# Kernel tuning notes

Hardware: AMD Instinct MI355X
Metric: run time of the kernel (lower is better)

The kernel has to match this reference:

```python
import jax, jax.numpy as jnp
import numpy as np

B, S, W, SYM, HID, ENT, ROLE, VOCAB, MAXSEQ = 256, 30, 10, 128, 512, 64, 32, 64, 16
LAYERS = 3
EPS = 1e-6


def setup_inputs() -> dict:
    key = jax.random.key(0)
    ks = jax.random.split(key, 16)
    rn = lambda i, shape, s: jax.random.normal(ks[i], shape, dtype=jnp.float32) * s
    inp = {
        'story': jax.random.randint(ks[0], (B, S, W), 0, VOCAB),
        'query': jax.random.randint(ks[1], (B, W), 0, VOCAB),
        'word_embed': rn(2, (VOCAB, SYM), 0.1),
        'pos_embed': jnp.ones((MAXSEQ, SYM), jnp.float32) / MAXSEQ,
        'ue_W1': rn(3, (2, SYM, HID), 0.05), 'ue_b1': jnp.zeros((2, HID), jnp.float32),
        'ue_W2': rn(4, (2, HID, ENT), 0.05), 'ue_b2': jnp.zeros((2, ENT), jnp.float32),
        'ur_W1': rn(5, (3, SYM, HID), 0.05), 'ur_b1': jnp.zeros((3, HID), jnp.float32),
        'ur_W2': rn(6, (3, HID, ROLE), 0.05), 'ur_b2': jnp.zeros((3, ROLE), jnp.float32),
        'fwm': rn(7, (ENT, ROLE, ENT), 0.08),
        'ie_W1': rn(8, (2, SYM, HID), 0.05), 'ie_b1': jnp.zeros((2, HID), jnp.float32),
        'ie_W2': rn(9, (2, HID, ENT), 0.05), 'ie_b2': jnp.zeros((2, ENT), jnp.float32),
        'ir_W1': rn(10, (3, SYM, HID), 0.05), 'ir_b1': jnp.zeros((3, HID), jnp.float32),
        'ir_W2': rn(11, (3, HID, ROLE), 0.05), 'ir_b2': jnp.zeros((3, ROLE), jnp.float32),
        'ln_gain': jnp.ones((3, ENT), jnp.float32),
        'ln_bias': jnp.zeros((3, ENT), jnp.float32),
        'Z': rn(12, (ENT, 9), 0.1),
    }
    return inp


def reference(story, query, word_embed, pos_embed,
              ue_W1, ue_b1, ue_W2, ue_b2, ur_W1, ur_b1, ur_W2, ur_b2, fwm,
              ie_W1, ie_b1, ie_W2, ie_b2, ir_W1, ir_b1, ir_W2, ir_b2,
              ln_gain, ln_bias, Z):
    # ---- InputModule: embed + position-weighted word sum ----
    sent = jnp.einsum('bswe,we->bse', word_embed[story], pos_embed[:story.shape[2]])  # [B,S,SYM]
    q = jnp.einsum('bwe,we->be', word_embed[query], pos_embed[:query.shape[1]])       # [B,SYM]

    # ---- UpdateModule: 2-layer tanh MLPs (stacked over head index n) ----
    h = jnp.tanh(jnp.einsum('bse,neh->nbsh', sent, ue_W1) + ue_b1[:, None, None, :])
    eo = jnp.tanh(jnp.einsum('nbsh,nho->nbso', h, ue_W2) + ue_b2[:, None, None, :])
    e1, e2 = eo[0], eo[1]                                                             # [B,S,ENT]
    h = jnp.tanh(jnp.einsum('bse,neh->nbsh', sent, ur_W1) + ur_b1[:, None, None, :])
    ro = jnp.tanh(jnp.einsum('nbsh,nho->nbso', h, ur_W2) + ur_b2[:, None, None, :])
    r1, r2, r3 = ro[0], ro[1], ro[2]                                                  # [B,S,ROLE]

    paw = jnp.einsum('bsr,bsf->bsrf', r1, e2)  # partial_add_w
    pab = jnp.einsum('bsr,bsf->bsrf', r3, e1)  # partial_add_b
    tpr = jnp.broadcast_to(fwm, (story.shape[0],) + fwm.shape)  # [B,ENT,ROLE,ENT]

    def step(tpr, _):
        w_hat = jnp.einsum('bse,bsr,berf->bsf', e1, r1, tpr)
        tpr = tpr + jnp.einsum('bse,bsrf->berf', e1, paw - jnp.einsum('bsr,bsf->bsrf', r1, w_hat))
        m_hat = jnp.einsum('bse,bsr,berf->bsf', e1, r2, tpr)
        move_op = jnp.einsum('bsr,bsf->bsrf', r2, w_hat) - jnp.einsum('bsr,bsf->bsrf', r2, m_hat)
        tpr = tpr + jnp.einsum('bse,bsrf->berf', e1, move_op)
        b_hat = jnp.einsum('bse,bsr,berf->bsf', e2, r3, tpr)
        tpr = tpr + jnp.einsum('bse,bsrf->berf', e2, pab - jnp.einsum('bsr,bsf->bsrf', r3, b_hat))
        fn = jnp.sqrt(jnp.sum(tpr * tpr, axis=(1, 2, 3)))
        fn = jax.nn.relu(fn - 1.0) + 1.0
        return tpr / fn[:, None, None, None], None

    tpr, _ = jax.lax.scan(step, tpr, None, length=LAYERS)

    # ---- InferenceModule ----
    h = jnp.tanh(jnp.einsum('be,neh->nbh', q, ie_W1) + ie_b1[:, None, :])
    qeo = jnp.tanh(jnp.einsum('nbh,nho->nbo', h, ie_W2) + ie_b2[:, None, :])
    qe1 = qeo[0]
    h = jnp.tanh(jnp.einsum('be,neh->nbh', q, ir_W1) + ir_b1[:, None, :])
    qro = jnp.tanh(jnp.einsum('nbh,nho->nbo', h, ir_W2) + ir_b2[:, None, :])
    qr1, qr2, qr3 = qro[0], qro[1], qro[2]

    def ln(x, i):
        m = jnp.mean(x, -1, keepdims=True)
        s = jnp.std(x, -1, keepdims=True, ddof=1)
        return ln_gain[i] * (x - m) / (s + EPS) + ln_bias[i]

    i1 = ln(jnp.einsum('be,br,berf->bf', qe1, qr1, tpr), 0)
    i2 = ln(jnp.einsum('be,br,berf->bf', i1, qr2, tpr), 1)
    i3 = ln(jnp.einsum('be,br,berf->bf', i2, qr3, tpr), 2)
    return jnp.einsum('bf,fl->bl', i1 + i2 + i3, Z)  # [B,9]
```

## Files before the change

### kernel.cpp

```cpp
#include <hip/hip_runtime.h>
#include <hip/hip_bf16.h>

#define NB 256
#define NS 30
#define NW 10
#define SYM 128
#define HID 512
#define ENT 64
#define ROLE 32

typedef unsigned short ushortT;
typedef __attribute__((ext_vector_type(8))) short short8v;
typedef __attribute__((ext_vector_type(4))) float f32x4;

static const size_t OF_SENTB = 0;
static const size_t OF_QEMBB = 491520;
static const size_t OF_W1A   = 507904;
static const size_t OF_W2TE  = 802816;
static const size_t OF_W2TR  = 851968;
static const size_t OF_FWMB  = 901120;
static const size_t OF_E1    = 966656;
static const size_t OF_R1    = 1949696;
static const size_t OF_QE1   = 2686976;
static const size_t OF_QR1   = 2703360;
static const size_t OF_PP    = 2727936;
static const size_t OF_FN2   = 4202496;
static const size_t OF_G     = 4202624;

__device__ __forceinline__ ushortT f2bf(float x) {
  unsigned u = __float_as_uint(x);
  unsigned r = (u + 0x7fffu + ((u >> 16) & 1u)) >> 16;
  return (ushortT)r;
}
__device__ __forceinline__ float ftanh(float x) {
  float t = __expf(2.f * x);
  return 1.f - 2.f * __builtin_amdgcn_rcpf(t + 1.f);
}
__device__ __forceinline__ float dot4(const float4& a, const float4& b) {
  return a.x * b.x + a.y * b.y + a.z * b.z + a.w * b.w;
}
__device__ __forceinline__ float wreduce64(float v) {
  #pragma unroll
  for (int o = 32; o > 0; o >>= 1) v += __shfl_xor(v, o);
  return v;
}

__global__ __launch_bounds__(256) void prep_k(
    const int* __restrict__ story, const int* __restrict__ query,
    const float* __restrict__ WE, const float* __restrict__ PE,
    const float* __restrict__ ueW1, const float* __restrict__ urW1,
    const float* __restrict__ ieW1, const float* __restrict__ irW1,
    const float* __restrict__ ueW2, const float* __restrict__ urW2,
    const float* __restrict__ ieW2, const float* __restrict__ irW2,
    const float* __restrict__ fwm,
    ushortT* __restrict__ sentb, ushortT* __restrict__ qembb,
    ushortT* __restrict__ W1A, ushortT* __restrict__ W2TE,
    ushortT* __restrict__ W2TR, ushortT* __restrict__ fwmBT,
    float* __restrict__ fn2) {
  __shared__ float tl[64 * 65];
  __shared__ float red[4];
  int bx = blockIdx.x, tid = threadIdx.x;
  if (bx < 3968) {
    int row = bx * 2 + (tid >> 7);
    int e = tid & 127;
    const int* idx; ushortT* dst;
    if (row < 7680) { idx = story + (size_t)row * NW; dst = sentb + (size_t)row * SYM; }
    else            { idx = query + (size_t)(row - 7680) * NW; dst = qembb + (size_t)(row - 7680) * SYM; }
    float acc = 0.f;
    #pragma unroll
    for (int w = 0; w < NW; ++w) acc += WE[idx[w] * SYM + e] * PE[w * SYM + e];
    dst[e] = f2bf(acc);
    return;
  }
  bx -= 3968;
  const float* src; ushortT* dst; int R, C, tr0, tc0;
  if (bx < 144) {
    int h = bx >> 4, t = bx & 15;
    src = (h < 2) ? ueW1 + (size_t)h * 65536 : (h < 5) ? urW1 + (size_t)(h - 2) * 65536
        : (h == 5) ? ieW1 : irW1 + (size_t)(h - 6) * 65536;
    dst = W1A + (size_t)h * 65536;
    R = 128; C = 512; tr0 = (t >> 3) * 64; tc0 = (t & 7) * 64;
  } else if (bx < 168) {
    int h = (bx - 144) >> 3, t = (bx - 144) & 7;
    src = (h < 2) ? ueW2 + (size_t)h * 32768 : ieW2;
    dst = W2TE + (size_t)h * 32768;
    R = 512; C = 64; tr0 = t * 64; tc0 = 0;
  } else if (bx < 216) {
    int h = (bx - 168) >> 3, t = (bx - 168) & 7;
    src = (h < 3) ? urW2 + (size_t)h * 16384 : irW2 + (size_t)(h - 3) * 16384;
    dst = W2TR + (size_t)h * 16384;
    R = 512; C = 32; tr0 = t * 64; tc0 = 0;
  } else if (bx < 248) {
    int t = bx - 216;
    src = fwm; dst = fwmBT; R = 2048; C = 64; tr0 = t * 64; tc0 = 0;
  } else {
    int blk = bx - 248;
    const float4* f4 = reinterpret_cast<const float4*>(fwm) + blk * 4096;
    float a = 0.f;
    for (int i = tid; i < 4096; i += 256) {
      float4 v = f4[i];
      a += v.x*v.x + v.y*v.y + v.z*v.z + v.w*v.w;
    }
    a = wreduce64(a);
    if ((tid & 63) == 0) red[tid >> 6] = a;
    __syncthreads();
    if (tid == 0) fn2[blk] = red[0] + red[1] + red[2] + red[3];
    return;
  }
  int TC = (C < 64) ? C : 64;
  int n = 64 * TC;
  for (int i = tid; i < n; i += 256) {
    int r = i / TC, c = i % TC;
    tl[r * 65 + c] = src[(size_t)(tr0 + r) * C + tc0 + c];
  }
  __syncthreads();
  for (int i = tid; i < n; i += 256) {
    int c = i >> 6, r = i & 63;
    dst[(size_t)(tc0 + c) * R + tr0 + r] = f2bf(tl[r * 65 + c]);
  }
}

__global__ __launch_bounds__(256, 4) void mlpm_k(
    const ushortT* __restrict__ sentB, const ushortT* __restrict__ qembB,
    const ushortT* __restrict__ W1A,
    const float* __restrict__ ueb1, const float* __restrict__ urb1,
    const float* __restrict__ ieb1, const float* __restrict__ irb1,
    const ushortT* __restrict__ W2TE, const ushortT* __restrict__ W2TR,
    const float* __restrict__ ueb2, const float* __restrict__ urb2,
    const float* __restrict__ ieb2, const float* __restrict__ irb2,
    float* __restrict__ E1, float* __restrict__ R1,
    float* __restrict__ QE1, float* __restrict__ QR1) {
  __shared__ __align__(16) ushortT Hl[32 * 520];
  int y = blockIdx.y;
  bool isQ = y >= 5;
  if (isQ && blockIdx.x >= 8) return;
  int r0 = blockIdx.x * 32, tid = threadIdx.x;
  int wave = tid >> 6, lane = tid & 63;
  int lrow = lane & 15;
  int kgrp = lane >> 4;
  const ushortT* Xb = isQ ? qembB : sentB;
  const ushortT* W1h = W1A + (size_t)y * 65536;
  const float* b1 = (y < 2) ? ueb1 + y * 512 : (y < 5) ? urb1 + (y - 2) * 512
                  : (y == 5) ? ieb1 : irb1 + (y - 6) * 512;
  bool isE = (y < 2) || (y == 5);

  int cw = wave * 128;

  short8v afr[2][4];
  #pragma unroll
  for (int rt = 0; rt < 2; ++rt) {
    const ushortT* arow = Xb + (size_t)(r0 + rt * 16 + lrow) * 128 + kgrp * 8;
    #pragma unroll
    for (int kt = 0; kt < 4; ++kt)
      afr[rt][kt] = *reinterpret_cast<const short8v*>(arow + kt * 32);
  }

  #pragma unroll
  for (int ct = 0; ct < 8; ++ct) {
    int c0 = cw + ct * 16;
    const ushortT* bcol = W1h + (size_t)(c0 + lrow) * 128 + kgrp * 8;
    short8v bf0 = *reinterpret_cast<const short8v*>(bcol);
    short8v bf1 = *reinterpret_cast<const short8v*>(bcol + 32);
    short8v bf2 = *reinterpret_cast<const short8v*>(bcol + 64);
    short8v bf3 = *reinterpret_cast<const short8v*>(bcol + 96);
    f32x4 aA[2] = {{0.f,0.f,0.f,0.f},{0.f,0.f,0.f,0.f}};
    f32x4 aB[2] = {{0.f,0.f,0.f,0.f},{0.f,0.f,0.f,0.f}};
    #pragma unroll
    for (int rt = 0; rt < 2; ++rt) {
      aA[rt] = __builtin_amdgcn_mfma_f32_16x16x32_bf16(afr[rt][0], bf0, aA[rt], 0, 0, 0);
      aB[rt] = __builtin_amdgcn_mfma_f32_16x16x32_bf16(afr[rt][1], bf1, aB[rt], 0, 0, 0);
      aA[rt] = __builtin_amdgcn_mfma_f32_16x16x32_bf16(afr[rt][2], bf2, aA[rt], 0, 0, 0);
      aB[rt] = __builtin_amdgcn_mfma_f32_16x16x32_bf16(afr[rt][3], bf3, aB[rt], 0, 0, 0);
    }
    int lcol = c0 + lrow;
    float bb = b1[lcol];
    #pragma unroll
    for (int rt = 0; rt < 2; ++rt)
      #pragma unroll
      for (int i = 0; i < 4; ++i) {
        float hv = ftanh(aA[rt][i] + aB[rt][i] + bb);
        Hl[(rt * 16 + kgrp * 4 + i) * 520 + lcol] = f2bf(hv);
      }
  }
  __syncthreads();

  if (isE) {
    int slot = (y == 5) ? 2 : y;
    const ushortT* W2h = W2TE + (size_t)slot * 32768;
    const float* b2 = (y == 5) ? ieb2 : ueb2 + y * 64;
    float* Out = (y == 5) ? QE1 : E1 + (size_t)y * 491520;
    int rt = wave >> 1, cb = (wave & 1) * 32;
    f32x4 accA[2] = {{0.f,0.f,0.f,0.f},{0.f,0.f,0.f,0.f}};
    f32x4 accB[2] = {{0.f,0.f,0.f,0.f},{0.f,0.f,0.f,0.f}};
    #pragma unroll
    for (int kt = 0; kt < 16; kt += 2) {
      int kb0 = kt * 32 + kgrp * 8;
      int kb1 = kb0 + 32;
      short8v a0 = *reinterpret_cast<const short8v*>(&Hl[(rt * 16 + lrow) * 520 + kb0]);
      short8v a1 = *reinterpret_cast<const short8v*>(&Hl[(rt * 16 + lrow) * 520 + kb1]);
      #pragma unroll
      for (int t = 0; t < 2; ++t) {
        const ushortT* wc = W2h + (size_t)(cb + t * 16 + lrow) * 512;
        short8v b0 = *reinterpret_cast<const short8v*>(wc + kb0);
        short8v b1v = *reinterpret_cast<const short8v*>(wc + kb1);
        accA[t] = __builtin_amdgcn_mfma_f32_16x16x32_bf16(a0, b0, accA[t], 0, 0, 0);
        accB[t] = __builtin_amdgcn_mfma_f32_16x16x32_bf16(a1, b1v, accB[t], 0, 0, 0);
      }
    }
    #pragma unroll
    for (int t = 0; t < 2; ++t) {
      int col = cb + t * 16 + lrow;
      float bb = b2[col];
      #pragma unroll
      for (int i = 0; i < 4; ++i) {
        int grow = r0 + rt * 16 + kgrp * 4 + i;
        Out[(size_t)grow * 64 + col] = ftanh(accA[t][i] + accB[t][i] + bb);
      }
    }
  } else {
    int slot = (y < 5) ? (y - 2) : (3 + y - 6);
    const ushortT* W2h = W2TR + (size_t)slot * 16384;
    const float* b2 = (y < 5) ? urb2 + (y - 2) * 32 : irb2 + (y - 6) * 32;
    float* Out = (y < 5) ? R1 + (size_t)(y - 2) * 245760 : QR1 + (size_t)(y - 6) * 8192;
    int rt = wave >> 1, cb = (wave & 1) * 16;
    f32x4 accA = {0.f, 0.f, 0.f, 0.f}, accB = {0.f, 0.f, 0.f, 0.f};
    const ushortT* wc = W2h + (size_t)(cb + lrow) * 512;
    #pragma unroll
    for (int kt = 0; kt < 16; kt += 2) {
      int kb0 = kt * 32 + kgrp * 8;
      int kb1 = kb0 + 32;
      short8v a0 = *reinterpret_cast<const short8v*>(&Hl[(rt * 16 + lrow) * 520 + kb0]);
      short8v a1 = *reinterpret_cast<const short8v*>(&Hl[(rt * 16 + lrow) * 520 + kb1]);
      short8v b0 = *reinterpret_cast<const short8v*>(wc + kb0);
      short8v b1v = *reinterpret_cast<const short8v*>(wc + kb1);
      accA = __builtin_amdgcn_mfma_f32_16x16x32_bf16(a0, b0, accA, 0, 0, 0);
      accB = __builtin_amdgcn_mfma_f32_16x16x32_bf16(a1, b1v, accB, 0, 0, 0);
    }
    int col = cb + lrow;
    float bb = b2[col];
    #pragma unroll
    for (int i = 0; i < 4; ++i) {
      int grow = r0 + rt * 16 + kgrp * 4 + i;
      Out[(size_t)grow * 32 + col] = ftanh(accA[i] + accB[i] + bb);
    }
  }
}

__global__ __launch_bounds__(256) void pstage_k(const ushortT* __restrict__ fwmBT,
    const float* __restrict__ e1g, const float* __restrict__ e2g,
    const float* __restrict__ r1g, const float* __restrict__ r2g, const float* __restrict__ r3g,
    const float* __restrict__ qr1g, const float* __restrict__ qr2g, const float* __restrict__ qr3g,
    float* __restrict__ Pp, float* __restrict__ Gg) {
  __shared__ __align__(16) float e1t[16 * 68], e2t[16 * 68];
  int bx = blockIdx.x, tid = threadIdx.x;
  int wave = tid >> 6, lane = tid & 63;
  int c = lane & 15, kg = lane >> 4;
  int f0 = wave * 16;
  const f32x4 zero = {0,0,0,0};

  if (bx >= 480) {
    int b = bx - 480;
    short8v qa = {0,0,0,0,0,0,0,0};
    if (c < 3) {
      const float* qr = ((c == 0) ? qr1g : (c == 1) ? qr2g : qr3g) + (size_t)b * 32 + kg * 8;
      ushortT* p = (ushortT*)&qa;
      #pragma unroll
      for (int j = 0; j < 8; ++j) p[j] = f2bf(qr[j]);
    }
    const ushortT* bbase = fwmBT + (size_t)(f0 + c) * 2048 + kg * 8;
    float* g0 = Gg + (size_t)b * 4096 + f0 + c;
    for (int e = 0; e < 64; ++e) {
      short8v B = *reinterpret_cast<const short8v*>(bbase + (size_t)e * 32);
      f32x4 T = __builtin_amdgcn_mfma_f32_16x16x32_bf16(qa, B, zero, 0, 0, 0);
      if (kg == 0) {
        g0[e * 64]           = T[0];
        g0[1048576 + e * 64] = T[1];
        g0[2097152 + e * 64] = T[2];
      }
    }
    return;
  }

  int rb = bx;
  {
    int row = tid >> 4, c4 = tid & 15;
    float4 v1 = *reinterpret_cast<const float4*>(e1g + ((size_t)rb * 16 + row) * 64 + c4 * 4);
    float4 v2 = *reinterpret_cast<const float4*>(e2g + ((size_t)rb * 16 + row) * 64 + c4 * 4);
    *reinterpret_cast<float4*>(&e1t[row * 68 + c4 * 4]) = v1;
    *reinterpret_cast<float4*>(&e2t[row * 68 + c4 * 4]) = v2;
  }
  size_t rbase = ((size_t)rb * 16 + c) * 32 + kg * 8;
  short8v rA, rB, rC;
  {
    float4 x0 = *reinterpret_cast<const float4*>(r1g + rbase);
    float4 x1 = *reinterpret_cast<const float4*>(r1g + rbase + 4);
    ushortT* p = (ushortT*)&rA;
    p[0]=f2bf(x0.x); p[1]=f2bf(x0.y); p[2]=f2bf(x0.z); p[3]=f2bf(x0.w);
    p[4]=f2bf(x1.x); p[5]=f2bf(x1.y); p[6]=f2bf(x1.z); p[7]=f2bf(x1.w);
    x0 = *reinterpret_cast<const float4*>(r2g + rbase);
    x1 = *reinterpret_cast<const float4*>(r2g + rbase + 4);
    p = (ushortT*)&rB;
    p[0]=f2bf(x0.x); p[1]=f2bf(x0.y); p[2]=f2bf(x0.z); p[3]=f2bf(x0.w);
    p[4]=f2bf(x1.x); p[5]=f2bf(x1.y); p[6]=f2bf(x1.z); p[7]=f2bf(x1.w);
    x0 = *reinterpret_cast<const float4*>(r3g + rbase);
    x1 = *reinterpret_cast<const float4*>(r3g + rbase + 4);
    p = (ushortT*)&rC;
    p[0]=f2bf(x0.x); p[1]=f2bf(x0.y); p[2]=f2bf(x0.z); p[3]=f2bf(x0.w);
    p[4]=f2bf(x1.x); p[5]=f2bf(x1.y); p[6]=f2bf(x1.z); p[7]=f2bf(x1.w);
  }
  __syncthreads();
  const ushortT* bbase = fwmBT + (size_t)(f0 + c) * 2048 + kg * 8;
  f32x4 P1 = {0,0,0,0}, P2 = {0,0,0,0}, P3 = {0,0,0,0};
  int r0 = kg * 4;
  for (int e4 = 0; e4 < 16; ++e4) {
    float4 ea[4], eb[4];
    #pragma unroll
    for (int i = 0; i < 4; ++i) {
      ea[i] = *reinterpret_cast<const float4*>(&e1t[(r0 + i) * 68 + e4 * 4]);
      eb[i] = *reinterpret_cast<const float4*>(&e2t[(r0 + i) * 68 + e4 * 4]);
    }
    #pragma unroll
    for (int sub = 0; sub < 4; ++sub) {
      int e = e4 * 4 + sub;
      short8v B = *reinterpret_cast<const short8v*>(bbase + (size_t)e * 32);
      f32x4 T1 = __builtin_amdgcn_mfma_f32_16x16x32_bf16(rA, B, zero, 0, 0, 0);
      f32x4 T2 = __builtin_amdgcn_mfma_f32_16x16x32_bf16(rB, B, zero, 0, 0, 0);
      f32x4 T3 = __builtin_amdgcn_mfma_f32_16x16x32_bf16(rC, B, zero, 0, 0, 0);
      #pragma unroll
      for (int i = 0; i < 4; ++i) {
        float e1v = reinterpret_cast<const float*>(&ea[i])[sub];
        float e2v = reinterpret_cast<const float*>(&eb[i])[sub];
        P1[i] += e1v * T1[i];
        P2[i] += e1v * T2[i];
        P3[i] += e2v * T3[i];
      }
    }
  }
  #pragma unroll
  for (int i = 0; i < 4; ++i) {
    size_t row = (size_t)rb * 16 + kg * 4 + i;
    Pp[row * 64 + f0 + c]               = P1[i];
    Pp[491520 + row * 64 + f0 + c]      = P2[i];
    Pp[2 * 491520 + row * 64 + f0 + c]  = P3[i];
  }
}

__global__ __launch_bounds__(1024) void scan_k(
    const float* __restrict__ Pp, const float* __restrict__ Gg,
    const float* __restrict__ e1g, const float* __restrict__ e2g,
    const float* __restrict__ r1g, const float* __restrict__ r2g, const float* __restrict__ r3g,
    const float* __restrict__ qe1g, const float* __restrict__ qr1g, const float* __restrict__ qr2g,
    const float* __restrict__ qr3g, const float* __restrict__ fn2p,
    const float* __restrict__ lng, const float* __restrict__ lnb, const float* __restrict__ Zg,
    float* __restrict__ out) {
  __shared__ __align__(16) float MPL[10800];
  __shared__ __align__(16) float e1L[2040], e2L[2040];
  __shared__ __align__(16) float v1L[2040], v2L[2040], v3L[2040];
  __shared__ __align__(16) float r1L[1080], r2L[1080], r3L[1080];
  __shared__ float uv[64], qv[96], alf[96], siL[64], rqL[272];
  __shared__ float redL[16];
  int b = blockIdx.x, tid = threadIdx.x;
  int s = tid >> 5, g = (tid >> 4) & 1, fo = tid & 15;
  int fq = fo * 4;
  bool act = s < 30;

  float H1[4], H2[4], H3[4], a1[4], a2[4], a3[4];
  #pragma unroll
  for (int j = 0; j < 4; ++j) { a1[j] = 0; a2[j] = 0; a3[j] = 0; }
  if (act) {
    size_t base = (size_t)b * 1920 + s * 64 + fq;
    float4 h1 = *reinterpret_cast<const float4*>(Pp + base);
    float4 h2 = *reinterpret_cast<const float4*>(Pp + 491520 + base);
    float4 h3 = *reinterpret_cast<const float4*>(Pp + 983040 + base);
    H1[0]=h1.x; H1[1]=h1.y; H1[2]=h1.z; H1[3]=h1.w;
    H2[0]=h2.x; H2[1]=h2.y; H2[2]=h2.z; H2[3]=h2.w;
    H3[0]=h3.x; H3[1]=h3.y; H3[2]=h3.z; H3[3]=h3.w;
  } else {
    #pragma unroll
    for (int j = 0; j < 4; ++j) { H1[j]=0; H2[j]=0; H3[j]=0; }
  }
  for (int i = tid; i < 1680; i += 1024) {
    if (i < 480) {
      int ss = i >> 4, c4 = i & 15;
      *reinterpret_cast<float4*>(&e1L[ss * 68 + c4 * 4]) =
          *reinterpret_cast<const float4*>(e1g + (size_t)b * 1920 + i * 4);
    } else if (i < 960) {
      int j = i - 480;
      int ss = j >> 4, c4 = j & 15;
      *reinterpret_cast<float4*>(&e2L[ss * 68 + c4 * 4]) =
          *reinterpret_cast<const float4*>(e2g + (size_t)b * 1920 + j * 4);
    } else {
      int j = i - 960;
      int which = j / 240, jj = j - which * 240;
      int ss = jj >> 3, c4 = jj & 7;
      float* dstL = (which == 0) ? r1L : (which == 1) ? r2L : r3L;
      const float* srcG = (which == 0) ? r1g : (which == 1) ? r2g : r3g;
      *reinterpret_cast<float4*>(&dstL[ss * 36 + c4 * 4]) =
          *reinterpret_cast<const float4*>(srcG + (size_t)b * 960 + jj * 4);
    }
  }
  if (tid >= 128 && tid < 224) {
    int t = tid - 128, st = t >> 5, k = t & 31;
    const float* qrg = (st == 0) ? qr1g : ((st == 1) ? qr2g : qr3g);
    qv[t] = qrg[(size_t)b * 32 + k];
  }
  __syncthreads();

  if (tid < 900) {
    int si = tid / 30, sj = tid - si * 30;
    float g11 = 0, g12 = 0, g21 = 0, g22 = 0;
    {
      const float4* A1 = reinterpret_cast<const float4*>(&e1L[si * 68]);
      const float4* A2 = reinterpret_cast<const float4*>(&e2L[si * 68]);
      const float4* C1 = reinterpret_cast<const float4*>(&e1L[sj * 68]);
      const float4* C2 = reinterpret_cast<const float4*>(&e2L[sj * 68]);
      #pragma unroll 4
      for (int i = 0; i < 16; ++i) {
        float4 a1v = A1[i], a2v = A2[i], c1v = C1[i], c2v = C2[i];
        g11 += dot4(a1v, c1v); g12 += dot4(a1v, c2v);
        g21 += dot4(a2v, c1v); g22 += dot4(a2v, c2v);
      }
    }
    float R11=0,R12=0,R13=0,R21=0,R22=0,R23=0,R31=0,R32=0,R33=0;
    {
      const float4* X1 = reinterpret_cast<const float4*>(&r1L[si * 36]);
      const float4* X2 = reinterpret_cast<const float4*>(&r2L[si * 36]);
      const float4* X3 = reinterpret_cast<const float4*>(&r3L[si * 36]);
      const float4* Y1 = reinterpret_cast<const float4*>(&r1L[sj * 36]);
      const float4* Y2 = reinterpret_cast<const float4*>(&r2L[sj * 36]);
      const float4* Y3 = reinterpret_cast<const float4*>(&r3L[sj * 36]);
      #pragma unroll 4
      for (int i = 0; i < 8; ++i) {
        float4 x1 = X1[i], x2 = X2[i], x3 = X3[i];
        float4 y1 = Y1[i], y2 = Y2[i], y3 = Y3[i];
        R11 += dot4(x1, y1); R12 += dot4(x1, y2); R13 += dot4(x1, y3);
        R21 += dot4(x2, y1); R22 += dot4(x2, y2); R23 += dot4(x2, y3);
        R31 += dot4(x3, y1); R32 += dot4(x3, y2); R33 += dot4(x3, y3);
      }
    }
    float4* MPv = reinterpret_cast<float4*>(MPL);
    float4 p1; p1.x = g11 * R11; p1.y = g11 * R21; p1.z = g21 * R31; p1.w = 0.f;
    float4 p2; p2.x = g11 * R12; p2.y = g11 * R22; p2.z = g21 * R32; p2.w = 0.f;
    float4 p3; p3.x = g12 * R13; p3.y = g12 * R23; p3.z = g22 * R33; p3.w = 0.f;
    MPv[tid] = p1;
    MPv[900 + tid] = p2;
    MPv[1800 + tid] = p3;
  } else {
    #pragma unroll
    for (int ch = 0; ch < 3; ++ch) {
      int t = (tid - 900) + ch * 124;
      if (t < 270) {
        int st = t / 90, rem = t - st * 90;
        int k = rem / 30, s2 = rem - k * 30;
        const float* rL = (k == 0) ? r1L : (k == 1) ? r2L : r3L;
        const float* qp = qv + st * 32;
        float a = 0.f;
        #pragma unroll 8
        for (int r = 0; r < 32; ++r) a += rL[s2 * 36 + r] * qp[r];
        rqL[st * 90 + k * 30 + s2] = a;
      }
    }
  }
  __syncthreads();

  float n2 = 0.f;
  #pragma unroll
  for (int i = 0; i < 8; ++i) n2 += fn2p[i];
  float c0v = 1.f;

  auto prop = [&](const float* vsrc, int mbase) {
    float d1[4] = {0,0,0,0}, d2[4] = {0,0,0,0}, d3[4] = {0,0,0,0};
    if (act) {
      const float4* mrow = reinterpret_cast<const float4*>(MPL) + mbase + s * 30 + g * 15;
      const float* vb = vsrc + g * 15 * 68 + fq;
      #pragma unroll 5
      for (int i = 0; i < 15; ++i) {
        float4 m = mrow[i];
        float4 vv = *reinterpret_cast<const float4*>(vb + i * 68);
        d1[0]+=m.x*vv.x; d1[1]+=m.x*vv.y; d1[2]+=m.x*vv.z; d1[3]+=m.x*vv.w;
        d2[0]+=m.y*vv.x; d2[1]+=m.y*vv.y; d2[2]+=m.y*vv.z; d2[3]+=m.y*vv.w;
        d3[0]+=m.z*vv.x; d3[1]+=m.z*vv.y; d3[2]+=m.z*vv.z; d3[3]+=m.z*vv.w;
      }
    }
    #pragma unroll
    for (int j = 0; j < 4; ++j) {
      H1[j] += d1[j] + __shfl_xor(d1[j], 16);
      H2[j] += d2[j] + __shfl_xor(d2[j], 16);
      H3[j] += d3[j] + __shfl_xor(d3[j], 16);
    }
  };

  for (int layer = 0; layer < 3; ++layer) {
    float w[4], H2s[4], H3s[4], v1r[4], v2r[4], v3r[4];
    if (act) {
      float4 e2v = *reinterpret_cast<const float4*>(&e2L[s * 68 + fq]);
      w[0]=H1[0]; w[1]=H1[1]; w[2]=H1[2]; w[3]=H1[3];
      #pragma unroll
      for (int j = 0; j < 4; ++j) { H2s[j] = H2[j]; H3s[j] = H3[j]; }
      v1r[0] = e2v.x - H1[0]; v1r[1] = e2v.y - H1[1]; v1r[2] = e2v.z - H1[2]; v1r[3] = e2v.w - H1[3];
      if (g == 0) {
        float4 t; t.x=v1r[0]; t.y=v1r[1]; t.z=v1r[2]; t.w=v1r[3];
        *reinterpret_cast<float4*>(&v1L[s * 68 + fq]) = t;
      }
    }
    __syncthreads();
    prop(v1L, 0);
    if (act) {
      #pragma unroll
      for (int j = 0; j < 4; ++j) v2r[j] = w[j] - H2[j];
      if (g == 0) {
        float4 t; t.x=v2r[0]; t.y=v2r[1]; t.z=v2r[2]; t.w=v2r[3];
        *reinterpret_cast<float4*>(&v2L[s * 68 + fq]) = t;
      }
    }
    __syncthreads();
    prop(v2L, 900);
    if (act) {
      float4 e1v = *reinterpret_cast<const float4*>(&e1L[s * 68 + fq]);
      v3r[0] = e1v.x - H3[0]; v3r[1] = e1v.y - H3[1]; v3r[2] = e1v.z - H3[2]; v3r[3] = e1v.w - H3[3];
      if (g == 0) {
        float4 t; t.x=v3r[0]; t.y=v3r[1]; t.z=v3r[2]; t.w=v3r[3];
        *reinterpret_cast<float4*>(&v3L[s * 68 + fq]) = t;
      }
    }
    __syncthreads();
    prop(v3L, 1800);
    float local = 0.f;
    if (act) {
      #pragma unroll
      for (int j = 0; j < 4; ++j) { a1[j] += v1r[j]; a2[j] += v2r[j]; a3[j] += v3r[j]; }
      if (g == 0) {
        #pragma unroll
        for (int j = 0; j < 4; ++j)
          local += v1r[j] * (w[j] + H1[j]) + v2r[j] * (H2s[j] + H2[j]) + v3r[j] * (H3s[j] + H3[j]);
      }
    }
    local = wreduce64(local);
    if ((tid & 63) == 0) redL[tid >> 6] = local;
    __syncthreads();
    float tot = n2;
    #pragma unroll
    for (int i = 0; i < 16; ++i) tot += redL[i];
    float fn = fmaxf(sqrtf(tot), 1.f);
    float inv = 1.f / fn;
    n2 = tot * inv * inv;
    c0v *= inv;
    if (act) {
      #pragma unroll
      for (int j = 0; j < 4; ++j) { H1[j]*=inv; H2[j]*=inv; H3[j]*=inv; a1[j]*=inv; a2[j]*=inv; a3[j]*=inv; }
    }
  }

  if (act && g == 0) {
    float4 t1; t1.x=a1[0]; t1.y=a1[1]; t1.z=a1[2]; t1.w=a1[3];
    float4 t2; t2.x=a2[0]; t2.y=a2[1]; t2.z=a2[2]; t2.w=a2[3];
    float4 t3; t3.x=a3[0]; t3.y=a3[1]; t3.z=a3[2]; t3.w=a3[3];
    *reinterpret_cast<float4*>(&v1L[s * 68 + fq]) = t1;
    *reinterpret_cast<float4*>(&v2L[s * 68 + fq]) = t2;
    *reinterpret_cast<float4*>(&v3L[s * 68 + fq]) = t3;
  }
  if (tid < 64) { uv[tid] = qe1g[(size_t)b * 64 + tid]; siL[tid] = 0.f; }
  __syncthreads();
  float* partL = MPL + 4096;
  int k32 = tid & 31;
  for (int st = 0; st < 3; ++st) {
    if (act) {
      float u0 = uv[k32], u1 = uv[k32 + 32];
      float eu1 = e1L[s * 68 + k32] * u0 + e1L[s * 68 + k32 + 32] * u1;
      float eu2 = e2L[s * 68 + k32] * u0 + e2L[s * 68 + k32 + 32] * u1;
      #pragma unroll
      for (int d = 16; d > 0; d >>= 1) {
        eu1 += __shfl_down(eu1, d, 32); eu2 += __shfl_down(eu2, d, 32);
      }
      if (k32 == 0) {
        alf[s]      = eu1 * rqL[st * 90 + s];
        alf[32 + s] = eu1 * rqL[st * 90 + 30 + s];
        alf[64 + s] = eu2 * rqL[st * 90 + 60 + s];
      }
    }
    __syncthreads();
    {
      int p = tid >> 6, f = tid & 63;
      float part = 0.f;
      if (p < 12) {
        int start = (p < 6) ? p * 3 : 18 + (p - 6) * 2;
        int cnt = (p < 6) ? 3 : 2;
        for (int q = 0; q < cnt; ++q) {
          int sp = start + q;
          part += alf[sp] * v1L[sp * 68 + f] + alf[32 + sp] * v2L[sp * 68 + f]
                + alf[64 + sp] * v3L[sp * 68 + f];
        }
      } else {
        int e0 = (p - 12) * 16;
        const float* Gp = Gg + (size_t)st * 1048576 + (size_t)b * 4096 + (size_t)e0 * 64 + f;
        float F = 0.f;
        #pragma unroll 4
        for (int e = 0; e < 16; ++e) F += uv[e0 + e] * Gp[e * 64];
        part = c0v * F;
      }
      partL[p * 64 + f] = part;
    }
    __syncthreads();
    if (tid < 64) {
      float raw = 0.f;
      #pragma unroll
      for (int p = 0; p < 16; ++p) raw += partL[p * 64 + tid];
      float mean = wreduce64(raw) * (1.f / 64.f);
      float d = raw - mean;
      float var = wreduce64(d * d) * (1.f / 63.f);
      float y = lng[st * 64 + tid] * d / (sqrtf(var) + 1e-6f) + lnb[st * 64 + tid];
      siL[tid] += y;
      uv[tid] = y;
    }
    __syncthreads();
  }
  if (tid < 9) {
    float o = 0.f;
    for (int ff = 0; ff < 64; ++ff) o += siL[ff] * Zg[ff * 9 + tid];
    out[(size_t)b * 9 + tid] = o;
  }
}

extern "C" void kernel_launch(void* const* d_in, const int* in_sizes, int n_in,
                              void* d_out, int out_size, void* d_ws, size_t ws_size,
                              hipStream_t stream) {
  const int*   story = (const int*)d_in[0];
  const int*   query = (const int*)d_in[1];
  const float* WE    = (const float*)d_in[2];
  const float* PE    = (const float*)d_in[3];
  const float* ueW1  = (const float*)d_in[4];
  const float* ueb1  = (const float*)d_in[5];
  const float* ueW2  = (const float*)d_in[6];
  const float* ueb2  = (const float*)d_in[7];
  const float* urW1  = (const float*)d_in[8];
  const float* urb1  = (const float*)d_in[9];
  const float* urW2  = (const float*)d_in[10];
  const float* urb2  = (const float*)d_in[11];
  const float* fwm   = (const float*)d_in[12];
  const float* ieW1  = (const float*)d_in[13];
  const float* ieb1  = (const float*)d_in[14];
  const float* ieW2  = (const float*)d_in[15];
  const float* ieb2  = (const float*)d_in[16];
  const float* irW1  = (const float*)d_in[17];
  const float* irb1  = (const float*)d_in[18];
  const float* irW2  = (const float*)d_in[19];
  const float* irb2  = (const float*)d_in[20];
  const float* lng   = (const float*)d_in[21];
  const float* lnb   = (const float*)d_in[22];
  const float* Z     = (const float*)d_in[23];
  float* W = (float*)d_ws;
  float* out = (float*)d_out;

  ushortT* sentB = (ushortT*)(W + OF_SENTB);
  ushortT* qembB = (ushortT*)(W + OF_QEMBB);
  ushortT* W1A   = (ushortT*)(W + OF_W1A);
  ushortT* W2TE  = (ushortT*)(W + OF_W2TE);
  ushortT* W2TR  = (ushortT*)(W + OF_W2TR);
  ushortT* fwmBT = (ushortT*)(W + OF_FWMB);

  prep_k<<<4232, 256, 0, stream>>>(story, query, WE, PE,
      ueW1, urW1, ieW1, irW1, ueW2, urW2, ieW2, irW2, fwm,
      sentB, qembB, W1A, W2TE, W2TR, fwmBT, W + OF_FN2);

  mlpm_k<<<dim3(240, 9), 256, 0, stream>>>(sentB, qembB, W1A,
      ueb1, urb1, ieb1, irb1, W2TE, W2TR, ueb2, urb2, ieb2, irb2,
      W + OF_E1, W + OF_R1, W + OF_QE1, W + OF_QR1);

  pstage_k<<<736, 256, 0, stream>>>(fwmBT, W + OF_E1, W + OF_E1 + 491520,
      W + OF_R1, W + OF_R1 + 245760, W + OF_R1 + 2 * 245760,
      W + OF_QR1, W + OF_QR1 + 8192, W + OF_QR1 + 16384,
      W + OF_PP, W + OF_G);

  scan_k<<<NB, 1024, 0, stream>>>(W + OF_PP, W + OF_G,
      W + OF_E1, W + OF_E1 + 491520,
      W + OF_R1, W + OF_R1 + 245760, W + OF_R1 + 2 * 245760,
      W + OF_QE1, W + OF_QR1, W + OF_QR1 + 8192, W + OF_QR1 + 16384,
      W + OF_FN2, lng, lnb, Z, out);
}
```

Measured before the change: 131.4 us.

## Move scan-layer propagation to split-bf16 MFMA with double-buffered LDS operands

The per-layer propagation matvecs in scan_k were FP32 FMA loops over a float4 M-matrix in shared memory. They are replaced by 16x16x32 bf16 MFMA using a hi/lo split (three MFMAs per product) to keep near-FP32 accuracy. The M matrices are padded to 32x40 and kept as bf16 hi/lo in LDS, with A fragments held in registers. Transposed v operands are double-buffered, and twelve waves each own one (k, row-tile, column-pair) slice. This targets the FP32 FMA cost of the serial 3-layer scan, at the price of extra conversion work and a possible precision change from bf16 splitting.

Result: faster. 115.1 us, median of 2 (-12.4%).

```diff
diff --git a/kernel.cpp b/kernel.cpp
--- a/kernel.cpp
+++ b/kernel.cpp
@@ -31,6 +31,9 @@
   unsigned u = __float_as_uint(x);
   unsigned r = (u + 0x7fffu + ((u >> 16) & 1u)) >> 16;
   return (ushortT)r;
+}
+__device__ __forceinline__ float bf2f(ushortT h) {
+  return __uint_as_float((unsigned)h << 16);
 }
 __device__ __forceinline__ float ftanh(float x) {
   float t = __expf(2.f * x);
@@ -353,32 +356,21 @@
     const float* __restrict__ qr3g, const float* __restrict__ fn2p,
     const float* __restrict__ lng, const float* __restrict__ lnb, const float* __restrict__ Zg,
     float* __restrict__ out) {
-  __shared__ __align__(16) float MPL[10800];
+  __shared__ __align__(16) ushortT MBs[2][9][1280];
+  __shared__ __align__(16) ushortT vTb[2][2][2560];
+  __shared__ float wLx[2048];
+  __shared__ float partBuf[1024];
   __shared__ __align__(16) float e1L[2040], e2L[2040];
   __shared__ __align__(16) float v1L[2040], v2L[2040], v3L[2040];
   __shared__ __align__(16) float r1L[1080], r2L[1080], r3L[1080];
   __shared__ float uv[64], qv[96], alf[96], siL[64], rqL[272];
   __shared__ float redL[16];
   int b = blockIdx.x, tid = threadIdx.x;
-  int s = tid >> 5, g = (tid >> 4) & 1, fo = tid & 15;
-  int fq = fo * 4;
-  bool act = s < 30;
-
-  float H1[4], H2[4], H3[4], a1[4], a2[4], a3[4];
-  #pragma unroll
-  for (int j = 0; j < 4; ++j) { a1[j] = 0; a2[j] = 0; a3[j] = 0; }
-  if (act) {
-    size_t base = (size_t)b * 1920 + s * 64 + fq;
-    float4 h1 = *reinterpret_cast<const float4*>(Pp + base);
-    float4 h2 = *reinterpret_cast<const float4*>(Pp + 491520 + base);
-    float4 h3 = *reinterpret_cast<const float4*>(Pp + 983040 + base);
-    H1[0]=h1.x; H1[1]=h1.y; H1[2]=h1.z; H1[3]=h1.w;
-    H2[0]=h2.x; H2[1]=h2.y; H2[2]=h2.z; H2[3]=h2.w;
-    H3[0]=h3.x; H3[1]=h3.y; H3[2]=h3.z; H3[3]=h3.w;
-  } else {
-    #pragma unroll
-    for (int j = 0; j < 4; ++j) { H1[j]=0; H2[j]=0; H3[j]=0; }
-  }
+  int wave = tid >> 6, lane = tid & 63;
+  int col = lane & 15, kgrp = lane >> 4;
+  bool wact = wave < 12;
+  int kk = wave >> 2, idx = wave & 3, st = idx >> 1, fp = idx & 1;
+
   for (int i = tid; i < 1680; i += 1024) {
     if (i < 480) {
       int ss = i >> 4, c4 = i & 15;
@@ -400,9 +392,29 @@
     }
   }
   if (tid >= 128 && tid < 224) {
-    int t = tid - 128, st = t >> 5, k = t & 31;
-    const float* qrg = (st == 0) ? qr1g : ((st == 1) ? qr2g : qr3g);
+    int t = tid - 128, sst = t >> 5, k = t & 31;
+    const float* qrg = (sst == 0) ? qr1g : ((sst == 1) ? qr2g : qr3g);
     qv[t] = qrg[(size_t)b * 32 + k];
+  }
+  for (int i = tid; i < 7200; i += 1024) {
+    int m = i / 400, rr = i - m * 400;
+    int hl = m / 9, mat = m - hl * 9;
+    int r, c;
+    if (rr < 320) { r = rr / 10; c = 30 + rr % 10; }
+    else { int q = rr - 320; r = 30 + q / 40; c = q % 40; }
+    MBs[hl][mat][r * 40 + c] = 0;
+  }
+  f32x4 Ht[2] = {{0.f,0.f,0.f,0.f},{0.f,0.f,0.f,0.f}};
+  float aT[2][4] = {{0,0,0,0},{0,0,0,0}};
+  if (wact) {
+    #pragma unroll
+    for (int t = 0; t < 2; ++t)
+      #pragma unroll
+      for (int i = 0; i < 4; ++i) {
+        int srow = st * 16 + kgrp * 4 + i;
+        int f = (fp * 2 + t) * 16 + col;
+        Ht[t][i] = (srow < 30) ? Pp[(size_t)kk * 491520 + (size_t)b * 1920 + srow * 64 + f] : 0.f;
+      }
   }
   __syncthreads();
 
@@ -438,102 +450,176 @@
         R31 += dot4(x3, y1); R32 += dot4(x3, y2); R33 += dot4(x3, y3);
       }
     }
-    float4* MPv = reinterpret_cast<float4*>(MPL);
-    float4 p1; p1.x = g11 * R11; p1.y = g11 * R21; p1.z = g21 * R31; p1.w = 0.f;
-    float4 p2; p2.x = g11 * R12; p2.y = g11 * R22; p2.z = g21 * R32; p2.w = 0.f;
-    float4 p3; p3.x = g12 * R13; p3.y = g12 * R23; p3.z = g22 * R33; p3.w = 0.f;
-    MPv[tid] = p1;
-    MPv[900 + tid] = p2;
-    MPv[1800 + tid] = p3;
+    float vals[9];
+    vals[0] = g11 * R11; vals[1] = g11 * R21; vals[2] = g21 * R31;
+    vals[3] = g11 * R12; vals[4] = g11 * R22; vals[5] = g21 * R32;
+    vals[6] = g12 * R13; vals[7] = g12 * R23; vals[8] = g22 * R33;
+    int o = si * 40 + sj;
+    #pragma unroll
+    for (int m = 0; m < 9; ++m) {
+      ushortT hi = f2bf(vals[m]);
+      float res = vals[m] - bf2f(hi);
+      MBs[0][m][o] = hi;
+      MBs[1][m][o] = f2bf(res);
+    }
   } else {
     #pragma unroll
     for (int ch = 0; ch < 3; ++ch) {
       int t = (tid - 900) + ch * 124;
       if (t < 270) {
-        int st = t / 90, rem = t - st * 90;
+        int sst = t / 90, rem = t - sst * 90;
         int k = rem / 30, s2 = rem - k * 30;
         const float* rL = (k == 0) ? r1L : (k == 1) ? r2L : r3L;
-        const float* qp = qv + st * 32;
+        const float* qp = qv + sst * 32;
         float a = 0.f;
         #pragma unroll 8
         for (int r = 0; r < 32; ++r) a += rL[s2 * 36 + r] * qp[r];
-        rqL[st * 90 + k * 30 + s2] = a;
-      }
-    }
+        rqL[sst * 90 + k * 30 + s2] = a;
+      }
+    }
+  }
+  float eP[2][4] = {{0,0,0,0},{0,0,0,0}};
+  if (wact && kk != 1) {
+    const float* eSrc = (kk == 0) ? e2L : e1L;
+    #pragma unroll
+    for (int t = 0; t < 2; ++t)
+      #pragma unroll
+      for (int i = 0; i < 4; ++i) {
+        int srow = st * 16 + kgrp * 4 + i;
+        if (srow < 30) eP[t][i] = eSrc[srow * 68 + (fp * 2 + t) * 16 + col];
+      }
   }
   __syncthreads();
+
+  short8v Ah0, Al0, Ah1, Al1, Ah2, Al2;
+  if (wact) {
+    int ao = (st * 16 + col) * 40 + kgrp * 8;
+    Ah0 = *reinterpret_cast<const short8v*>(&MBs[0][kk][ao]);
+    Al0 = *reinterpret_cast<const short8v*>(&MBs[1][kk][ao]);
+    Ah1 = *reinterpret_cast<const short8v*>(&MBs[0][3 + kk][ao]);
+    Al1 = *reinterpret_cast<const short8v*>(&MBs[1][3 + kk][ao]);
+    Ah2 = *reinterpret_cast<const short8v*>(&MBs[0][6 + kk][ao]);
+    Al2 = *reinterpret_cast<const short8v*>(&MBs[1][6 + kk][ao]);
+  }
 
   float n2 = 0.f;
   #pragma unroll
   for (int i = 0; i < 8; ++i) n2 += fn2p[i];
   float c0v = 1.f;
 
-  auto prop = [&](const float* vsrc, int mbase) {
-    float d1[4] = {0,0,0,0}, d2[4] = {0,0,0,0}, d3[4] = {0,0,0,0};
-    if (act) {
-      const float4* mrow = reinterpret_cast<const float4*>(MPL) + mbase + s * 30 + g * 15;
-      const float* vb = vsrc + g * 15 * 68 + fq;
-      #pragma unroll 5
-      for (int i = 0; i < 15; ++i) {
-        float4 m = mrow[i];
-        float4 vv = *reinterpret_cast<const float4*>(vb + i * 68);
-        d1[0]+=m.x*vv.x; d1[1]+=m.x*vv.y; d1[2]+=m.x*vv.z; d1[3]+=m.x*vv.w;
-        d2[0]+=m.y*vv.x; d2[1]+=m.y*vv.y; d2[2]+=m.y*vv.z; d2[3]+=m.y*vv.w;
-        d3[0]+=m.z*vv.x; d3[1]+=m.z*vv.y; d3[2]+=m.z*vv.z; d3[3]+=m.z*vv.w;
-      }
-    }
-    #pragma unroll
-    for (int j = 0; j < 4; ++j) {
-      H1[j] += d1[j] + __shfl_xor(d1[j], 16);
-      H2[j] += d2[j] + __shfl_xor(d2[j], 16);
-      H3[j] += d3[j] + __shfl_xor(d3[j], 16);
+  float sav[2][4], vr[2][4];
+  auto vWrite = [&](int bsel) {
+    #pragma unroll
+    for (int t = 0; t < 2; ++t) {
+      ushortT h0 = f2bf(vr[t][0]), h1 = f2bf(vr[t][1]), h2 = f2bf(vr[t][2]), h3 = f2bf(vr[t][3]);
+      float r0 = vr[t][0] - bf2f(h0), r1 = vr[t][1] - bf2f(h1);
+      float r2 = vr[t][2] - bf2f(h2), r3 = vr[t][3] - bf2f(h3);
+      uint2 hw, lw;
+      hw.x = (unsigned)h0 | ((unsigned)h1 << 16);
+      hw.y = (unsigned)h2 | ((unsigned)h3 << 16);
+      lw.x = (unsigned)f2bf(r0) | ((unsigned)f2bf(r1) << 16);
+      lw.y = (unsigned)f2bf(r2) | ((unsigned)f2bf(r3) << 16);
+      int off = ((fp * 2 + t) * 16 + col) * 40 + st * 16 + kgrp * 4;
+      *reinterpret_cast<uint2*>(&vTb[bsel][0][off]) = hw;
+      *reinterpret_cast<uint2*>(&vTb[bsel][1][off]) = lw;
     }
   };
-
+  auto mfmaPh = [&](int bsel, short8v AH, short8v AL) {
+    if (wact) {
+      #pragma unroll
+      for (int t = 0; t < 2; ++t) {
+        int off = ((fp * 2 + t) * 16 + col) * 40 + kgrp * 8;
+        short8v Bh = *reinterpret_cast<const short8v*>(&vTb[bsel][0][off]);
+        short8v Bl = *reinterpret_cast<const short8v*>(&vTb[bsel][1][off]);
+        Ht[t] = __builtin_amdgcn_mfma_f32_16x16x32_bf16(AH, Bh, Ht[t], 0, 0, 0);
+        Ht[t] = __builtin_amdgcn_mfma_f32_16x16x32_bf16(AH, Bl, Ht[t], 0, 0, 0);
+        Ht[t] = __builtin_amdgcn_mfma_f32_16x16x32_bf16(AL, Bh, Ht[t], 0, 0, 0);
+      }
+    }
+  };
+
+  int buf = 0;
   for (int layer = 0; layer < 3; ++layer) {
-    float w[4], H2s[4], H3s[4], v1r[4], v2r[4], v3r[4];
-    if (act) {
-      float4 e2v = *reinterpret_cast<const float4*>(&e2L[s * 68 + fq]);
-      w[0]=H1[0]; w[1]=H1[1]; w[2]=H1[2]; w[3]=H1[3];
-      #pragma unroll
-      for (int j = 0; j < 4; ++j) { H2s[j] = H2[j]; H3s[j] = H3[j]; }
-      v1r[0] = e2v.x - H1[0]; v1r[1] = e2v.y - H1[1]; v1r[2] = e2v.z - H1[2]; v1r[3] = e2v.w - H1[3];
-      if (g == 0) {
-        float4 t; t.x=v1r[0]; t.y=v1r[1]; t.z=v1r[2]; t.w=v1r[3];
-        *reinterpret_cast<float4*>(&v1L[s * 68 + fq]) = t;
-      }
+    if (wact) {
+      #pragma unroll
+      for (int t = 0; t < 2; ++t)
+        #pragma unroll
+        for (int i = 0; i < 4; ++i) { sav[t][i] = Ht[t][i]; vr[t][i] = 0.f; }
+      if (kk == 0) {
+        int base = idx * 512 + lane * 8;
+        #pragma unroll
+        for (int t = 0; t < 2; ++t)
+          #pragma unroll
+          for (int i = 0; i < 4; ++i) wLx[base + t * 4 + i] = Ht[t][i];
+      }
+    }
+    if (wact && kk == 0) {
+      #pragma unroll
+      for (int t = 0; t < 2; ++t)
+        #pragma unroll
+        for (int i = 0; i < 4; ++i) {
+          int srow = st * 16 + kgrp * 4 + i;
+          vr[t][i] = (srow < 30) ? (eP[t][i] - Ht[t][i]) : 0.f;
+        }
+      vWrite(buf);
     }
     __syncthreads();
-    prop(v1L, 0);
-    if (act) {
-      #pragma unroll
-      for (int j = 0; j < 4; ++j) v2r[j] = w[j] - H2[j];
-      if (g == 0) {
-        float4 t; t.x=v2r[0]; t.y=v2r[1]; t.z=v2r[2]; t.w=v2r[3];
-        *reinterpret_cast<float4*>(&v2L[s * 68 + fq]) = t;
-      }
+    mfmaPh(buf, Ah0, Al0);
+    buf ^= 1;
+    if (wact && kk == 0) {
+      #pragma unroll
+      for (int t = 0; t < 2; ++t)
+        #pragma unroll
+        for (int i = 0; i < 4; ++i) aT[t][i] += vr[t][i];
+    }
+    if (wact && kk == 1) {
+      int base = idx * 512 + lane * 8;
+      #pragma unroll
+      for (int t = 0; t < 2; ++t)
+        #pragma unroll
+        for (int i = 0; i < 4; ++i) {
+          int srow = st * 16 + kgrp * 4 + i;
+          vr[t][i] = (srow < 30) ? (wLx[base + t * 4 + i] - Ht[t][i]) : 0.f;
+        }
+      vWrite(buf);
     }
     __syncthreads();
-    prop(v2L, 900);
-    if (act) {
-      float4 e1v = *reinterpret_cast<const float4*>(&e1L[s * 68 + fq]);
-      v3r[0] = e1v.x - H3[0]; v3r[1] = e1v.y - H3[1]; v3r[2] = e1v.z - H3[2]; v3r[3] = e1v.w - H3[3];
-      if (g == 0) {
-        float4 t; t.x=v3r[0]; t.y=v3r[1]; t.z=v3r[2]; t.w=v3r[3];
-        *reinterpret_cast<float4*>(&v3L[s * 68 + fq]) = t;
-      }
+    mfmaPh(buf, Ah1, Al1);
+    buf ^= 1;
+    if (wact && kk == 1) {
+      #pragma unroll
+      for (int t = 0; t < 2; ++t)
+        #pragma unroll
+        for (int i = 0; i < 4; ++i) aT[t][i] += vr[t][i];
+    }
+    if (wact && kk == 2) {
+      #pragma unroll
+      for (int t = 0; t < 2; ++t)
+        #pragma unroll
+        for (int i = 0; i < 4; ++i) {
+          int srow = st * 16 + kgrp * 4 + i;
+          vr[t][i] = (srow < 30) ? (eP[t][i] - Ht[t][i]) : 0.f;
+        }
+      vWrite(buf);
     }
     __syncthreads();
-    prop(v3L, 1800);
+    mfmaPh(buf, Ah2, Al2);
+    buf ^= 1;
+    if (wact && kk == 2) {
+      #pragma unroll
+      for (int t = 0; t < 2; ++t)
+        #pragma unroll
+        for (int i = 0; i < 4; ++i) aT[t][i] += vr[t][i];
+    }
     float local = 0.f;
-    if (act) {
-      #pragma unroll
-      for (int j = 0; j < 4; ++j) { a1[j] += v1r[j]; a2[j] += v2r[j]; a3[j] += v3r[j]; }
-      if (g == 0) {
-        #pragma unroll
-        for (int j = 0; j < 4; ++j)
-          local += v1r[j] * (w[j] + H1[j]) + v2r[j] * (H2s[j] + H2[j]) + v3r[j] * (H3s[j] + H3[j]);
-      }
+    if (wact) {
+      #pragma unroll
+      for (int t = 0; t < 2; ++t)
+        #pragma unroll
+        for (int i = 0; i < 4; ++i) {
+          int srow = st * 16 + kgrp * 4 + i;
+          if (srow < 30) local += vr[t][i] * (sav[t][i] + Ht[t][i]);
+        }
     }
     local = wreduce64(local);
     if ((tid & 63) == 0) redL[tid >> 6] = local;
@@ -545,25 +631,32 @@
     float inv = 1.f / fn;
     n2 = tot * inv * inv;
     c0v *= inv;
-    if (act) {
-      #pragma unroll
-      for (int j = 0; j < 4; ++j) { H1[j]*=inv; H2[j]*=inv; H3[j]*=inv; a1[j]*=inv; a2[j]*=inv; a3[j]*=inv; }
-    }
-  }
-
-  if (act && g == 0) {
-    float4 t1; t1.x=a1[0]; t1.y=a1[1]; t1.z=a1[2]; t1.w=a1[3];
-    float4 t2; t2.x=a2[0]; t2.y=a2[1]; t2.z=a2[2]; t2.w=a2[3];
-    float4 t3; t3.x=a3[0]; t3.y=a3[1]; t3.z=a3[2]; t3.w=a3[3];
-    *reinterpret_cast<float4*>(&v1L[s * 68 + fq]) = t1;
-    *reinterpret_cast<float4*>(&v2L[s * 68 + fq]) = t2;
-    *reinterpret_cast<float4*>(&v3L[s * 68 + fq]) = t3;
+    if (wact) {
+      #pragma unroll
+      for (int t = 0; t < 2; ++t)
+        #pragma unroll
+        for (int i = 0; i < 4; ++i) { Ht[t][i] *= inv; aT[t][i] *= inv; }
+    }
+  }
+
+  if (wact) {
+    float* dstA = (kk == 0) ? v1L : (kk == 1) ? v2L : v3L;
+    #pragma unroll
+    for (int t = 0; t < 2; ++t)
+      #pragma unroll
+      for (int i = 0; i < 4; ++i) {
+        int srow = st * 16 + kgrp * 4 + i;
+        if (srow < 30) dstA[srow * 68 + (fp * 2 + t) * 16 + col] = aT[t][i];
+      }
   }
   if (tid < 64) { uv[tid] = qe1g[(size_t)b * 64 + tid]; siL[tid] = 0.f; }
   __syncthreads();
-  float* partL = MPL + 4096;
+
+  int s = tid >> 5;
+  bool act = s < 30;
+  float* partL = partBuf;
   int k32 = tid & 31;
-  for (int st = 0; st < 3; ++st) {
+  for (int stg = 0; stg < 3; ++stg) {
     if (act) {
       float u0 = uv[k32], u1 = uv[k32 + 32];
       float eu1 = e1L[s * 68 + k32] * u0 + e1L[s * 68 + k32 + 32] * u1;
@@ -573,9 +666,9 @@
         eu1 += __shfl_down(eu1, d, 32); eu2 += __shfl_down(eu2, d, 32);
       }
       if (k32 == 0) {
-        alf[s]      = eu1 * rqL[st * 90 + s];
-        alf[32 + s] = eu1 * rqL[st * 90 + 30 + s];
-        alf[64 + s] = eu2 * rqL[st * 90 + 60 + s];
+        alf[s]      = eu1 * rqL[stg * 90 + s];
+        alf[32 + s] = eu1 * rqL[stg * 90 + 30 + s];
+        alf[64 + s] = eu2 * rqL[stg * 90 + 60 + s];
       }
     }
     __syncthreads();
@@ -592,7 +685,7 @@
         }
       } else {
         int e0 = (p - 12) * 16;
-        const float* Gp = Gg + (size_t)st * 1048576 + (size_t)b * 4096 + (size_t)e0 * 64 + f;
+        const float* Gp = Gg + (size_t)stg * 1048576 + (size_t)b * 4096 + (size_t)e0 * 64 + f;
         float F = 0.f;
         #pragma unroll 4
         for (int e = 0; e < 16; ++e) F += uv[e0 + e] * Gp[e * 64];
@@ -608,7 +701,7 @@
       float mean = wreduce64(raw) * (1.f / 64.f);
       float d = raw - mean;
       float var = wreduce64(d * d) * (1.f / 63.f);
-      float y = lng[st * 64 + tid] * d / (sqrtf(var) + 1e-6f) + lnb[st * 64 + tid];
+      float y = lng[stg * 64 + tid] * d / (sqrtf(var) + 1e-6f) + lnb[stg * 64 + tid];
       siL[tid] += y;
       uv[tid] = y;
     }
```
